# Performance work log

Hardware: AMD Instinct MI355X
Metric: run time of the kernel (lower is better)

## Reference

```python
import jax, jax.numpy as jnp
import numpy as np

B, NQ, NK, C, H = 4, 1024, 1024, 768, 12
DH = C // H
SCALE = DH ** -0.5
EPS = 1e-5  # nn.LayerNorm default
NEG_INF = float('-inf')


def _ln(x, g, b):
    m = jnp.mean(x, axis=-1, keepdims=True)
    v = jnp.mean((x - m) ** 2, axis=-1, keepdims=True)
    return (x - m) * jax.lax.rsqrt(v + EPS) * g + b


def _heads(t):  # [B,N,C] -> [B,H,N,Dh]
    Bq, N, _ = t.shape
    return t.reshape(Bq, N, H, DH).transpose(0, 2, 1, 3)


def setup_inputs() -> dict:
    key = jax.random.key(0)
    ks = jax.random.split(key, 32)
    w = lambda k, shape: jax.random.normal(k, shape, jnp.float32) * 0.02
    g = lambda k: 1.0 + jax.random.normal(k, (C,), jnp.float32) * 0.02
    b = lambda k: jax.random.normal(k, (C,), jnp.float32) * 0.02
    inp = {
        'x': jax.random.normal(ks[0], (B, NQ, C), jnp.float32),
        'y': jax.random.normal(ks[1], (B, NK, C), jnp.float32),
        'xpos': jnp.arange(B * NQ, dtype=jnp.int32).reshape(B, NQ),
        'ypos': jnp.arange(B * NK, dtype=jnp.int32).reshape(B, NK),
        'mask': jax.random.randint(ks[2], (NQ, NK), 0, 2) > 0,
        'similarities': jax.random.normal(ks[3], (B, H, NQ, NK), jnp.float32),
        # norms
        'ln1_g': g(ks[4]), 'ln1_b': b(ks[5]),
        'ln2_g': g(ks[6]), 'ln2_b': b(ks[7]),
        'ln3_g': g(ks[8]), 'ln3_b': b(ks[9]),
        'lny_g': g(ks[10]), 'lny_b': b(ks[11]),
        # self-attn (qkv_bias=False)
        'qkv_w': w(ks[12], (3 * C, C)),
        'aproj_w': w(ks[13], (C, C)), 'aproj_b': b(ks[14]),
        # cross-attn
        'pq_w': w(ks[15], (C, C)), 'pk_w': w(ks[16], (C, C)), 'pv_w': w(ks[17], (C, C)),
        'cproj_w': w(ks[18], (C, C)), 'cproj_b': b(ks[19]),
        # mlp (hidden = 4*C)
        'fc1_w': w(ks[20], (4 * C, C)), 'fc1_b': jax.random.normal(ks[21], (4 * C,), jnp.float32) * 0.02,
        'fc2_w': w(ks[22], (C, 4 * C)), 'fc2_b': b(ks[23]),
    }
    return inp


def reference(x, y, xpos, ypos, mask, similarities,
              ln1_g, ln1_b, ln2_g, ln2_b, ln3_g, ln3_b, lny_g, lny_b,
              qkv_w, aproj_w, aproj_b,
              pq_w, pk_w, pv_w, cproj_w, cproj_b,
              fc1_w, fc1_b, fc2_w, fc2_b):
    # ---- self-attention (rope=None, dropout=0) ----
    xn = _ln(x, ln1_g, ln1_b)
    qkv = (xn @ qkv_w.T).reshape(B, NQ, 3, H, DH).transpose(2, 0, 3, 1, 4)
    q, k, v = qkv[0], qkv[1], qkv[2]                       # [B,H,Nq,Dh]
    attn = jax.nn.softmax(jnp.einsum('bhqd,bhkd->bhqk', q, k) * SCALE, axis=-1)
    sa = jnp.einsum('bhqk,bhkd->bhqd', attn, v).transpose(0, 2, 1, 3).reshape(B, NQ, C)
    x = x + sa @ aproj_w.T + aproj_b

    # ---- sparse cross-attention with similarity bias + mask ----
    y_ = _ln(y, lny_g, lny_b)
    xn2 = _ln(x, ln2_g, ln2_b)
    cq = _heads(xn2 @ pq_w.T)                              # [B,H,Nq,Dh]
    ck = _heads(y_ @ pk_w.T)                               # [B,H,Nk,Dh]
    cv = _heads(y_ @ pv_w.T)
    scores = jnp.einsum('bhqd,bhkd->bhqk', cq, ck) * SCALE
    sims_c = similarities - jnp.mean(similarities, axis=1, keepdims=True)
    scores = scores + sims_c
    scores = jnp.where(mask[None, None], scores, NEG_INF)
    cattn = jax.nn.softmax(scores, axis=-1)
    ca = jnp.einsum('bhqk,bhkd->bhqd', cattn, cv).transpose(0, 2, 1, 3).reshape(B, NQ, C)
    x = x + ca @ cproj_w.T + cproj_b

    # ---- MLP (exact GELU, as nn.GELU default) ----
    xn3 = _ln(x, ln3_g, ln3_b)
    h = jax.nn.gelu(xn3 @ fc1_w.T + fc1_b, approximate=False)
    x = x + h @ fc2_w.T + fc2_b
    return (x, y)
```

## Files before the change

kernel.cpp:

```cpp
#include <hip/hip_runtime.h>
#include <cstdint>
#include <cstddef>


typedef __bf16 bf16;
typedef __attribute__((ext_vector_type(8))) __bf16 bf16x8;
typedef __attribute__((ext_vector_type(4))) __bf16 bf16x4;
typedef __attribute__((ext_vector_type(4))) float f32x4;

typedef __attribute__((address_space(1))) void gvoid;
typedef __attribute__((address_space(3))) void lvoid;

#define DEVI static __device__ __forceinline__

DEVI void gload16(const void* g, void* l) {
  __builtin_amdgcn_global_load_lds((gvoid*)(uintptr_t)g, (lvoid*)(uintptr_t)l, 16, 0, 0);
}

DEVI f32x4 mfma_bf16(bf16x8 a, bf16x8 b, f32x4 c) {
  return __builtin_amdgcn_mfma_f32_16x16x32_bf16(a, b, c, 0, 0, 0);
}

__global__ __launch_bounds__(256)
void bias_k(const float* __restrict__ sim,
            const unsigned char* __restrict__ mask,
            bf16* __restrict__ biasOut)
{
  __shared__ int red[4];
  const int blk = blockIdx.x;
  const int b = blk >> 10, q = blk & 1023;
  const int t = threadIdx.x;
  const int k4 = t * 4;

  int ds = mask[t * 4 + 1] + mask[t * 4 + 2] + mask[t * 4 + 3];
  #pragma unroll
  for (int o = 32; o; o >>= 1) ds += __shfl_xor(ds, o);
  if ((t & 63) == 0) red[t >> 6] = ds;
  __syncthreads();
  const int msh = ((red[0] + red[1] + red[2] + red[3]) == 0) ? 2 : 0;

  const float* sb = sim + (size_t)b * 12 * 1024 * 1024;
  bf16* ob = biasOut + (size_t)b * 12 * 1024 * 1024;

  f32x4 sv[12];
  f32x4 acc = {0.f, 0.f, 0.f, 0.f};
  #pragma unroll
  for (int h = 0; h < 12; ++h) {
    sv[h] = *(const f32x4*)(sb + ((size_t)h * 1024 + q) * 1024 + k4);
    acc += sv[h];
  }
  const f32x4 mean = acc * (1.0f / 12.0f);

  float mb[4];
  if (msh == 0) {
    const uchar4 mv = *(const uchar4*)(mask + (size_t)q * 1024 + k4);
    mb[0] = mv.x ? 0.f : -1e30f; mb[1] = mv.y ? 0.f : -1e30f;
    mb[2] = mv.z ? 0.f : -1e30f; mb[3] = mv.w ? 0.f : -1e30f;
  } else {
    const int4 mv = *(const int4*)((const int*)mask + (size_t)q * 1024 + k4);
    mb[0] = mv.x ? 0.f : -1e30f; mb[1] = mv.y ? 0.f : -1e30f;
    mb[2] = mv.z ? 0.f : -1e30f; mb[3] = mv.w ? 0.f : -1e30f;
  }

  #pragma unroll
  for (int h = 0; h < 12; ++h) {
    bf16x4 o;
    #pragma unroll
    for (int j = 0; j < 4; ++j)
      o[j] = (bf16)(sv[h][j] - mean[j] + mb[j]);
    *(bf16x4*)(ob + ((size_t)h * 1024 + q) * 1024 + k4) = o;
  }
}

struct CvtArgs {
  const float* src[8];
  bf16* dst[8];
  int end[8];
};
__global__ __launch_bounds__(256)
void cvt_all_k(CvtArgs a)
{
  const int i = blockIdx.x * 256 + threadIdx.x;
  int s = 0;
  #pragma unroll
  for (int j = 0; j < 7; ++j) s += (i >= a.end[j]) ? 1 : 0;
  const int base = s ? a.end[s - 1] : 0;
  const int off = i - base;
  const f32x4 v = *((const f32x4*)a.src[s] + off);
  bf16x4 o;
  o[0] = (bf16)v[0]; o[1] = (bf16)v[1]; o[2] = (bf16)v[2]; o[3] = (bf16)v[3];
  *(bf16x4*)(a.dst[s] + (size_t)off * 4) = o;
}

__global__ __launch_bounds__(256)
void copy4_k(const float* __restrict__ s, float* __restrict__ d, int n4)
{
  const int i = blockIdx.x * 256 + threadIdx.x;
  if (i < n4) ((f32x4*)d)[i] = ((const f32x4*)s)[i];
}

template<bool DUAL>
__global__ __launch_bounds__(256)
void ln_k(const float* __restrict__ inA, const float* __restrict__ gA,
          const float* __restrict__ bA, bf16* __restrict__ outA,
          const float* __restrict__ inB, const float* __restrict__ gB,
          const float* __restrict__ bB, bf16* __restrict__ outB)
{
  int row = blockIdx.x;
  const float* xin = inA; const float* g = gA; const float* be = bA; bf16* out = outA;
  if constexpr (DUAL) {
    if (row >= 4096) {
      row -= 4096; xin = inB; g = gB; be = bB; out = outB;
    }
  }
  const int tid = threadIdx.x;
  const int lane = tid & 63, w = tid >> 6;
  const float* xr = xin + (size_t)row * 768;
  const float v0 = xr[tid], v1 = xr[tid + 256], v2 = xr[tid + 512];
  float s = v0 + v1 + v2;
  #pragma unroll
  for (int o = 32; o; o >>= 1) s += __shfl_xor(s, o);
  __shared__ float r1[4], r2[4];
  if (lane == 0) r1[w] = s;
  __syncthreads();
  const float mean = (r1[0] + r1[1] + r1[2] + r1[3]) * (1.0f / 768.0f);
  const float d0 = v0 - mean, d1 = v1 - mean, d2 = v2 - mean;
  float q = d0 * d0 + d1 * d1 + d2 * d2;
  #pragma unroll
  for (int o = 32; o; o >>= 1) q += __shfl_xor(q, o);
  if (lane == 0) r2[w] = q;
  __syncthreads();
  const float inv = rsqrtf((r2[0] + r2[1] + r2[2] + r2[3]) * (1.0f / 768.0f) + 1e-5f);
  bf16* orow = out + (size_t)row * 768;
  orow[tid]       = (bf16)(d0 * inv * g[tid]       + be[tid]);
  orow[tid + 256] = (bf16)(d1 * inv * g[tid + 256] + be[tid + 256]);
  orow[tid + 512] = (bf16)(d2 * inv * g[tid + 512] + be[tid + 512]);
}

template<int BM, int BN, bool BIAS, bool GELU, bool RES, bool OBF, bool VT>
__global__ __launch_bounds__(256)
void gemm_bt(const bf16* __restrict__ A, const bf16* __restrict__ Bt,
             const float* __restrict__ bias, const float* __restrict__ res,
             bf16* __restrict__ Cb, float* __restrict__ Cf,
             bf16* __restrict__ vtOut, int vtBase,
             int nyPerXcd, int N, int K)
{
  constexpr int WM = BM / 2, WN = BN / 2;
  constexpr int FM = WM / 16, FN = WN / 16;
  __shared__ bf16 As[BM * 64];
  __shared__ bf16 Bs[BN * 64];
  const int f = blockIdx.x;
  const int xcd = f & 7, j = f >> 3;
  const int by = xcd + 8 * (j % nyPerXcd);
  const int bx = j / nyPerXcd;
  const int tid = threadIdx.x;
  const int lane = tid & 63;
  const int wv = tid >> 6;
  const int wr = wv >> 1, wc = wv & 1;
  const int l15 = lane & 15, lg = lane >> 4;
  const int bm = by * BM, bn = bx * BN;

  f32x4 acc[FM][FN];
  const f32x4 z = {0.f, 0.f, 0.f, 0.f};
  #pragma unroll
  for (int i = 0; i < FM; ++i)
    #pragma unroll
    for (int jj = 0; jj < FN; ++jj) acc[i][jj] = z;

  for (int k0 = 0; k0 < K; k0 += 64) {
    __syncthreads();
    #pragma unroll
    for (int c = tid; c < BM * 8; c += 256) {
      const int row = c >> 3, colb = (c & 7) << 4;
      gload16((const char*)A + ((size_t)(bm + row) * K + k0) * 2 + colb,
              (char*)As + (size_t)c * 16);
    }
    #pragma unroll
    for (int c = tid; c < BN * 8; c += 256) {
      const int row = c >> 3, colb = (c & 7) << 4;
      gload16((const char*)Bt + ((size_t)(bn + row) * K + k0) * 2 + colb,
              (char*)Bs + (size_t)c * 16);
    }
    __syncthreads();
    #pragma unroll
    for (int kk = 0; kk < 64; kk += 32) {
      bf16x8 af[FM], bfr[FN];
      #pragma unroll
      for (int mi = 0; mi < FM; ++mi)
        af[mi] = *(const bf16x8*)(As + (size_t)(wr * WM + mi * 16 + l15) * 64 + kk + lg * 8);
      #pragma unroll
      for (int ni = 0; ni < FN; ++ni)
        bfr[ni] = *(const bf16x8*)(Bs + (size_t)(wc * WN + ni * 16 + l15) * 64 + kk + lg * 8);
      #pragma unroll
      for (int mi = 0; mi < FM; ++mi)
        #pragma unroll
        for (int ni = 0; ni < FN; ++ni)
          acc[mi][ni] = mfma_bf16(af[mi], bfr[ni], acc[mi][ni]);
    }
  }

  #pragma unroll
  for (int mi = 0; mi < FM; ++mi) {
    const int row0 = bm + wr * WM + mi * 16 + lg * 4;
    #pragma unroll
    for (int ni = 0; ni < FN; ++ni) {
      const int col = bn + wc * WN + ni * 16 + l15;
      if constexpr (VT) {
        if (col >= vtBase) {
          const int hd = col - vtBase;
          const int bb = row0 >> 10, n0 = row0 & 1023;
          bf16x4 ov;
          #pragma unroll
          for (int r = 0; r < 4; ++r) ov[r] = (bf16)acc[mi][ni][r];
          *(bf16x4*)(vtOut + ((size_t)(bb * 768 + hd)) * 1024 + n0) = ov;
          continue;
        }
      }
      #pragma unroll
      for (int r = 0; r < 4; ++r) {
        float v = acc[mi][ni][r];
        if constexpr (BIAS) v += bias[col];
        if constexpr (GELU) v = 0.5f * v * (1.0f + erff(v * 0.70710678118654752f));
        if constexpr (RES)  v += res[(size_t)(row0 + r) * N + col];
        if constexpr (OBF)  Cb[(size_t)(row0 + r) * N + col] = (bf16)v;
        else                Cf[(size_t)(row0 + r) * N + col] = v;
      }
    }
  }
}

template<int CROSS>
__global__ __launch_bounds__(256, 3)
void fattn_k(const bf16* __restrict__ Qp, int ldq,
             const bf16* __restrict__ Kp, int ldk,
             const bf16* __restrict__ Vt,
             const bf16* __restrict__ bias,
             bf16* __restrict__ Out)
{
  __shared__ bf16 Kl[2][64 * 64];
  __shared__ bf16 Vl[2][64 * 64];
  __shared__ bf16 Pl[4][16 * 72];

  const int f = blockIdx.x;
  const int r8 = f & 7, rest = f >> 3;
  const int c6 = rest % 6, qt = rest / 6;
  const int pp = r8 + 8 * c6;
  const int b = pp / 12, hh = pp % 12;
  const int tid = threadIdx.x, lane = tid & 63, wq = tid >> 6;
  const int l15 = lane & 15, lg = lane >> 4;

  bf16x8 qreg0, qreg1;
  {
    const bf16* qsrc = Qp + (size_t)(b * 1024 + qt * 64 + wq * 16 + l15) * ldq + hh * 64 + lg * 8;
    qreg0 = *(const bf16x8*)qsrc;
    qreg1 = *(const bf16x8*)(qsrc + 32);
  }
  const char* Kbase = (const char*)(Kp + (size_t)b * 1024 * ldk + hh * 64);
  const char* Vbase = (const char*)(Vt + (size_t)(b * 12 + hh) * 64 * 1024);
  const bf16* biasRow = nullptr;
  if constexpr (CROSS)
    biasRow = bias + (((size_t)(b * 12 + hh)) * 1024 + qt * 64 + wq * 16 + l15) * 1024;

  f32x4 oacc[4];
  const f32x4 z = {0.f, 0.f, 0.f, 0.f};
  #pragma unroll
  for (int i = 0; i < 4; ++i) oacc[i] = z;
  float m_run = -1e30f, l_run = 0.f;

  char* PlW = (char*)&Pl[wq][0];
  const int swz = (l15 & 7) << 4;

  auto stage = [&](int buf, int t) {
    const int k0 = t * 64;
    #pragma unroll
    for (int jj = 0; jj < 2; ++jj) {
      const int c = jj * 256 + tid;
      const int r = c >> 3;
      const int sw = ((c & 7) ^ (r & 7)) << 4;
      gload16(Kbase + ((size_t)(k0 + r) * ldk) * 2 + sw, (char*)&Kl[buf][0] + (size_t)c * 16);
      gload16(Vbase + (size_t)r * 2048 + (size_t)k0 * 2 + sw, (char*)&Vl[buf][0] + (size_t)c * 16);
    }
  };

  stage(0, 0);
  __syncthreads();

  for (int t = 0; t < 16; ++t) {
    const int cur = t & 1;
    const int k0 = t * 64;
    if (t < 15) stage(cur ^ 1, t + 1);

    bf16x4 bv[4];
    if constexpr (CROSS) {
      const bf16* bp = biasRow + k0 + lg * 4;
      #pragma unroll
      for (int ni = 0; ni < 4; ++ni) bv[ni] = *(const bf16x4*)(bp + ni * 16);
    }

    f32x4 sacc[4];
    #pragma unroll
    for (int i = 0; i < 4; ++i) sacc[i] = z;
    #pragma unroll
    for (int ni = 0; ni < 4; ++ni) {
      const int rowb = (ni * 16 + l15) * 128;
      const bf16x8 a0 = *(const bf16x8*)((char*)&Kl[cur][0] + rowb + ((lg * 16) ^ swz));
      const bf16x8 a1 = *(const bf16x8*)((char*)&Kl[cur][0] + rowb + ((64 + lg * 16) ^ swz));
      sacc[ni] = mfma_bf16(a0, qreg0, sacc[ni]);
      sacc[ni] = mfma_bf16(a1, qreg1, sacc[ni]);
    }

    float sv[16];
    #pragma unroll
    for (int ni = 0; ni < 4; ++ni)
      #pragma unroll
      for (int r = 0; r < 4; ++r)
        sv[ni * 4 + r] = sacc[ni][r] * 0.125f;
    if constexpr (CROSS) {
      #pragma unroll
      for (int ni = 0; ni < 4; ++ni)
        #pragma unroll
        for (int r = 0; r < 4; ++r)
          sv[ni * 4 + r] += (float)bv[ni][r];
    }
    float mx = sv[0];
    #pragma unroll
    for (int jj = 1; jj < 16; ++jj) mx = fmaxf(mx, sv[jj]);
    mx = fmaxf(mx, __shfl_xor(mx, 16));
    mx = fmaxf(mx, __shfl_xor(mx, 32));
    const float mnew = fmaxf(m_run, mx);
    const float corr = __expf(m_run - mnew);
    m_run = mnew;
    float ps = 0.f;
    #pragma unroll
    for (int jj = 0; jj < 16; ++jj) { sv[jj] = __expf(sv[jj] - mnew); ps += sv[jj]; }
    l_run = l_run * corr + ps;

    #pragma unroll
    for (int ni = 0; ni < 4; ++ni) {
      bf16x4 pw;
      #pragma unroll
      for (int r = 0; r < 4; ++r) pw[r] = (bf16)sv[ni * 4 + r];
      *(bf16x4*)(PlW + l15 * 144 + ni * 32 + lg * 8) = pw;
    }
    float cr[4];
    #pragma unroll
    for (int r = 0; r < 4; ++r) cr[r] = __shfl(corr, ((lane >> 4) << 2) + r);
    #pragma unroll
    for (int nd = 0; nd < 4; ++nd)
      #pragma unroll
      for (int r = 0; r < 4; ++r) oacc[nd][r] *= cr[r];

    const bf16x8 p0 = *(const bf16x8*)(PlW + l15 * 144 + lg * 16);
    const bf16x8 p1 = *(const bf16x8*)(PlW + l15 * 144 + 64 + lg * 16);
    #pragma unroll
    for (int nd = 0; nd < 4; ++nd) {
      const int rowb = (nd * 16 + l15) * 128;
      const bf16x8 v0 = *(const bf16x8*)((char*)&Vl[cur][0] + rowb + ((lg * 16) ^ swz));
      const bf16x8 v1 = *(const bf16x8*)((char*)&Vl[cur][0] + rowb + ((64 + lg * 16) ^ swz));
      oacc[nd] = mfma_bf16(p0, v0, oacc[nd]);
      oacc[nd] = mfma_bf16(p1, v1, oacc[nd]);
    }
    __syncthreads();
  }

  float ls = l_run + __shfl_xor(l_run, 16);
  ls += __shfl_xor(ls, 32);
  const float inv = 1.0f / ls;
  float ivr[4];
  #pragma unroll
  for (int r = 0; r < 4; ++r) ivr[r] = __shfl(inv, ((lane >> 4) << 2) + r);
  bf16* ob = Out + (size_t)(b * 1024 + qt * 64 + wq * 16 + lg * 4) * 768 + hh * 64 + l15;
  #pragma unroll
  for (int r = 0; r < 4; ++r)
    #pragma unroll
    for (int nd = 0; nd < 4; ++nd)
      ob[(size_t)r * 768 + nd * 16] = (bf16)(oacc[nd][r] * ivr[r]);
}

extern "C" void kernel_launch(void* const* d_in, const int* in_sizes, int n_in,
                              void* d_out, int out_size, void* d_ws, size_t ws_size,
                              hipStream_t stream)
{
  (void)in_sizes; (void)n_in; (void)out_size; (void)ws_size;
  const float* x    = (const float*)d_in[0];
  const float* y    = (const float*)d_in[1];
  const unsigned char* mask = (const unsigned char*)d_in[4];
  const float* sim  = (const float*)d_in[5];
  const float* ln1g = (const float*)d_in[6];
  const float* ln1b = (const float*)d_in[7];
  const float* ln2g = (const float*)d_in[8];
  const float* ln2b = (const float*)d_in[9];
  const float* ln3g = (const float*)d_in[10];
  const float* ln3b = (const float*)d_in[11];
  const float* lnyg = (const float*)d_in[12];
  const float* lnyb = (const float*)d_in[13];
  const float* qkvw = (const float*)d_in[14];
  const float* apw  = (const float*)d_in[15];
  const float* apb  = (const float*)d_in[16];
  const float* pqw  = (const float*)d_in[17];
  const float* pkw  = (const float*)d_in[18];
  const float* pvw  = (const float*)d_in[19];
  const float* cpw  = (const float*)d_in[20];
  const float* cpb  = (const float*)d_in[21];
  const float* f1w  = (const float*)d_in[22];
  const float* f1b  = (const float*)d_in[23];
  const float* f2w  = (const float*)d_in[24];
  const float* f2b  = (const float*)d_in[25];

  char* ws = (char*)d_ws;
  size_t off = 0;
  auto alloc = [&](size_t bytes) -> void* {
    off = (off + 255) & ~(size_t)255;
    void* p = ws + off;
    off += bytes;
    return p;
  };
  const size_t T = 4096;
  bf16* w_qkv = (bf16*)alloc((size_t)2304 * 768 * 2);
  bf16* w_ap  = (bf16*)alloc((size_t)768 * 768 * 2);
  bf16* w_pq  = (bf16*)alloc((size_t)768 * 768 * 2);
  bf16* w_pkv = (bf16*)alloc((size_t)1536 * 768 * 2);
  bf16* w_cp  = (bf16*)alloc((size_t)768 * 768 * 2);
  bf16* w_f1  = (bf16*)alloc((size_t)3072 * 768 * 2);
  bf16* w_f2  = (bf16*)alloc((size_t)768 * 3072 * 2);
  bf16* xn    = (bf16*)alloc(T * 768 * 2);
  bf16* qkvo  = (bf16*)alloc(T * 2304 * 2);
  bf16* vt    = (bf16*)alloc((size_t)48 * 64 * 1024 * 2);
  bf16* sa    = (bf16*)alloc(T * 768 * 2);
  float* x1   = (float*)alloc(T * 768 * 4);
  bf16* yln   = (bf16*)alloc(T * 768 * 2);
  bf16* xn2   = (bf16*)alloc(T * 768 * 2);
  bf16* cqf   = (bf16*)alloc(T * 768 * 2);
  bf16* ckv   = (bf16*)alloc(T * 1536 * 2);
  bf16* cvtT  = (bf16*)alloc((size_t)48 * 64 * 1024 * 2);
  bf16* biasA = (bf16*)alloc((size_t)4 * 12 * 1024 * 1024 * 2);
  bf16* ca    = (bf16*)alloc(T * 768 * 2);
  float* x2   = (float*)alloc(T * 768 * 4);
  bf16* xn3   = (bf16*)alloc(T * 768 * 2);
  bf16* hbuf  = (bf16*)alloc(T * 3072 * 2);

  {
    CvtArgs a;
    const float* srcs[8] = {qkvw, apw, pqw, pkw, pvw, cpw, f1w, f2w};
    bf16* dsts[8] = {w_qkv, w_ap, w_pq, w_pkv, w_pkv + 768 * 768, w_cp, w_f1, w_f2};
    const int n4s[8] = {442368, 147456, 147456, 147456, 147456, 147456, 589824, 589824};
    int cum = 0;
    for (int j = 0; j < 8; ++j) {
      a.src[j] = srcs[j]; a.dst[j] = dsts[j];
      cum += n4s[j]; a.end[j] = cum;
    }
    cvt_all_k<<<cum / 256, 256, 0, stream>>>(a);
  }

  bias_k<<<4096, 256, 0, stream>>>(sim, mask, biasA);

  ln_k<true><<<8192, 256, 0, stream>>>(x, ln1g, ln1b, xn, y, lnyg, lnyb, yln);
  gemm_bt<128,128,false,false,false,true,true><<<576, 256, 0, stream>>>(
      xn, w_qkv, nullptr, nullptr, qkvo, nullptr, vt, 1536, 4, 2304, 768);
  fattn_k<0><<<768, 256, 0, stream>>>(
      qkvo, 2304, qkvo + 768, 2304, vt, nullptr, sa);
  gemm_bt<64,128,true,false,true,false,false><<<384, 256, 0, stream>>>(
      sa, w_ap, apb, x, nullptr, x1, nullptr, 0, 8, 768, 768);

  ln_k<false><<<4096, 256, 0, stream>>>(x1, ln2g, ln2b, xn2,
                                        nullptr, nullptr, nullptr, nullptr);
  gemm_bt<64,128,false,false,false,true,false><<<384, 256, 0, stream>>>(
      xn2, w_pq, nullptr, nullptr, cqf, nullptr, nullptr, 0, 8, 768, 768);
  gemm_bt<128,128,false,false,false,true,true><<<384, 256, 0, stream>>>(
      yln, w_pkv, nullptr, nullptr, ckv, nullptr, cvtT, 768, 4, 1536, 768);
  fattn_k<1><<<768, 256, 0, stream>>>(
      cqf, 768, ckv, 1536, cvtT, biasA, ca);
  gemm_bt<64,128,true,false,true,false,false><<<384, 256, 0, stream>>>(
      ca, w_cp, cpb, x1, nullptr, x2, nullptr, 0, 8, 768, 768);

  ln_k<false><<<4096, 256, 0, stream>>>(x2, ln3g, ln3b, xn3,
                                        nullptr, nullptr, nullptr, nullptr);
  gemm_bt<128,128,true,true,false,true,false><<<768, 256, 0, stream>>>(
      xn3, w_f1, f1b, nullptr, hbuf, nullptr, nullptr, 0, 4, 3072, 768);
  gemm_bt<64,128,true,false,true,false,false><<<384, 256, 0, stream>>>(
      hbuf, w_f2, f2b, x2, nullptr, (float*)d_out, nullptr, 0, 8, 768, 3072);

  copy4_k<<<3072, 256, 0, stream>>>(y, (float*)d_out + 3145728, 786432);
}
```

Measured before the change: 388.6 us.

## Merge independent kernels into combined launches to fill the GPU

Several independent kernels now share a launch, with branches on block index. Weight conversion and both LayerNorms run as one prep kernel, the QKV GEMM runs alongside the similarity-bias kernel, the attention projection GEMM runs with the K/V projection GEMM, and FC2 runs with the y copy. The aim is to cut launch count and fill the tail of small-grid GEMMs with other independent work. The cost is heterogeneous blocks and a shared-memory size set by the largest branch, which may lower occupancy for the lighter blocks.

```diff
diff --git a/kernel.cpp b/kernel.cpp
--- a/kernel.cpp
+++ b/kernel.cpp
@@ -21,138 +21,16 @@
   return __builtin_amdgcn_mfma_f32_16x16x32_bf16(a, b, c, 0, 0, 0);
 }
 
-__global__ __launch_bounds__(256)
-void bias_k(const float* __restrict__ sim,
-            const unsigned char* __restrict__ mask,
-            bf16* __restrict__ biasOut)
-{
-  __shared__ int red[4];
-  const int blk = blockIdx.x;
-  const int b = blk >> 10, q = blk & 1023;
-  const int t = threadIdx.x;
-  const int k4 = t * 4;
-
-  int ds = mask[t * 4 + 1] + mask[t * 4 + 2] + mask[t * 4 + 3];
-  #pragma unroll
-  for (int o = 32; o; o >>= 1) ds += __shfl_xor(ds, o);
-  if ((t & 63) == 0) red[t >> 6] = ds;
-  __syncthreads();
-  const int msh = ((red[0] + red[1] + red[2] + red[3]) == 0) ? 2 : 0;
-
-  const float* sb = sim + (size_t)b * 12 * 1024 * 1024;
-  bf16* ob = biasOut + (size_t)b * 12 * 1024 * 1024;
-
-  f32x4 sv[12];
-  f32x4 acc = {0.f, 0.f, 0.f, 0.f};
-  #pragma unroll
-  for (int h = 0; h < 12; ++h) {
-    sv[h] = *(const f32x4*)(sb + ((size_t)h * 1024 + q) * 1024 + k4);
-    acc += sv[h];
-  }
-  const f32x4 mean = acc * (1.0f / 12.0f);
-
-  float mb[4];
-  if (msh == 0) {
-    const uchar4 mv = *(const uchar4*)(mask + (size_t)q * 1024 + k4);
-    mb[0] = mv.x ? 0.f : -1e30f; mb[1] = mv.y ? 0.f : -1e30f;
-    mb[2] = mv.z ? 0.f : -1e30f; mb[3] = mv.w ? 0.f : -1e30f;
-  } else {
-    const int4 mv = *(const int4*)((const int*)mask + (size_t)q * 1024 + k4);
-    mb[0] = mv.x ? 0.f : -1e30f; mb[1] = mv.y ? 0.f : -1e30f;
-    mb[2] = mv.z ? 0.f : -1e30f; mb[3] = mv.w ? 0.f : -1e30f;
-  }
-
-  #pragma unroll
-  for (int h = 0; h < 12; ++h) {
-    bf16x4 o;
-    #pragma unroll
-    for (int j = 0; j < 4; ++j)
-      o[j] = (bf16)(sv[h][j] - mean[j] + mb[j]);
-    *(bf16x4*)(ob + ((size_t)h * 1024 + q) * 1024 + k4) = o;
-  }
-}
-
-struct CvtArgs {
-  const float* src[8];
-  bf16* dst[8];
-  int end[8];
-};
-__global__ __launch_bounds__(256)
-void cvt_all_k(CvtArgs a)
-{
-  const int i = blockIdx.x * 256 + threadIdx.x;
-  int s = 0;
-  #pragma unroll
-  for (int j = 0; j < 7; ++j) s += (i >= a.end[j]) ? 1 : 0;
-  const int base = s ? a.end[s - 1] : 0;
-  const int off = i - base;
-  const f32x4 v = *((const f32x4*)a.src[s] + off);
-  bf16x4 o;
-  o[0] = (bf16)v[0]; o[1] = (bf16)v[1]; o[2] = (bf16)v[2]; o[3] = (bf16)v[3];
-  *(bf16x4*)(a.dst[s] + (size_t)off * 4) = o;
-}
-
-__global__ __launch_bounds__(256)
-void copy4_k(const float* __restrict__ s, float* __restrict__ d, int n4)
-{
-  const int i = blockIdx.x * 256 + threadIdx.x;
-  if (i < n4) ((f32x4*)d)[i] = ((const f32x4*)s)[i];
-}
-
-template<bool DUAL>
-__global__ __launch_bounds__(256)
-void ln_k(const float* __restrict__ inA, const float* __restrict__ gA,
-          const float* __restrict__ bA, bf16* __restrict__ outA,
-          const float* __restrict__ inB, const float* __restrict__ gB,
-          const float* __restrict__ bB, bf16* __restrict__ outB)
-{
-  int row = blockIdx.x;
-  const float* xin = inA; const float* g = gA; const float* be = bA; bf16* out = outA;
-  if constexpr (DUAL) {
-    if (row >= 4096) {
-      row -= 4096; xin = inB; g = gB; be = bB; out = outB;
-    }
-  }
-  const int tid = threadIdx.x;
-  const int lane = tid & 63, w = tid >> 6;
-  const float* xr = xin + (size_t)row * 768;
-  const float v0 = xr[tid], v1 = xr[tid + 256], v2 = xr[tid + 512];
-  float s = v0 + v1 + v2;
-  #pragma unroll
-  for (int o = 32; o; o >>= 1) s += __shfl_xor(s, o);
-  __shared__ float r1[4], r2[4];
-  if (lane == 0) r1[w] = s;
-  __syncthreads();
-  const float mean = (r1[0] + r1[1] + r1[2] + r1[3]) * (1.0f / 768.0f);
-  const float d0 = v0 - mean, d1 = v1 - mean, d2 = v2 - mean;
-  float q = d0 * d0 + d1 * d1 + d2 * d2;
-  #pragma unroll
-  for (int o = 32; o; o >>= 1) q += __shfl_xor(q, o);
-  if (lane == 0) r2[w] = q;
-  __syncthreads();
-  const float inv = rsqrtf((r2[0] + r2[1] + r2[2] + r2[3]) * (1.0f / 768.0f) + 1e-5f);
-  bf16* orow = out + (size_t)row * 768;
-  orow[tid]       = (bf16)(d0 * inv * g[tid]       + be[tid]);
-  orow[tid + 256] = (bf16)(d1 * inv * g[tid + 256] + be[tid + 256]);
-  orow[tid + 512] = (bf16)(d2 * inv * g[tid + 512] + be[tid + 512]);
-}
 
 template<int BM, int BN, bool BIAS, bool GELU, bool RES, bool OBF, bool VT>
-__global__ __launch_bounds__(256)
-void gemm_bt(const bf16* __restrict__ A, const bf16* __restrict__ Bt,
-             const float* __restrict__ bias, const float* __restrict__ res,
-             bf16* __restrict__ Cb, float* __restrict__ Cf,
-             bf16* __restrict__ vtOut, int vtBase,
-             int nyPerXcd, int N, int K)
+DEVI void gemm_dev(bf16* As, bf16* Bs, int by, int bx,
+                   const bf16* __restrict__ A, const bf16* __restrict__ Bt,
+                   const float* __restrict__ bias, const float* __restrict__ res,
+                   bf16* __restrict__ Cb, float* __restrict__ Cf,
+                   bf16* __restrict__ vtOut, int vtBase, int N, int K)
 {
   constexpr int WM = BM / 2, WN = BN / 2;
   constexpr int FM = WM / 16, FN = WN / 16;
-  __shared__ bf16 As[BM * 64];
-  __shared__ bf16 Bs[BN * 64];
-  const int f = blockIdx.x;
-  const int xcd = f & 7, j = f >> 3;
-  const int by = xcd + 8 * (j % nyPerXcd);
-  const int bx = j / nyPerXcd;
   const int tid = threadIdx.x;
   const int lane = tid & 63;
   const int wv = tid >> 6;
@@ -227,6 +105,208 @@
       }
     }
   }
+}
+
+DEVI void bias_dev(int blk, int* red,
+                   const float* __restrict__ sim,
+                   const unsigned char* __restrict__ mask,
+                   bf16* __restrict__ biasOut)
+{
+  const int b = blk >> 10, q = blk & 1023;
+  const int t = threadIdx.x;
+  const int k4 = t * 4;
+
+  int ds = mask[t * 4 + 1] + mask[t * 4 + 2] + mask[t * 4 + 3];
+  #pragma unroll
+  for (int o = 32; o; o >>= 1) ds += __shfl_xor(ds, o);
+  if ((t & 63) == 0) red[t >> 6] = ds;
+  __syncthreads();
+  const int msh = ((red[0] + red[1] + red[2] + red[3]) == 0) ? 2 : 0;
+
+  const float* sb = sim + (size_t)b * 12 * 1024 * 1024;
+  bf16* ob = biasOut + (size_t)b * 12 * 1024 * 1024;
+
+  f32x4 sv[12];
+  f32x4 acc = {0.f, 0.f, 0.f, 0.f};
+  #pragma unroll
+  for (int h = 0; h < 12; ++h) {
+    sv[h] = *(const f32x4*)(sb + ((size_t)h * 1024 + q) * 1024 + k4);
+    acc += sv[h];
+  }
+  const f32x4 mean = acc * (1.0f / 12.0f);
+
+  float mb[4];
+  if (msh == 0) {
+    const uchar4 mv = *(const uchar4*)(mask + (size_t)q * 1024 + k4);
+    mb[0] = mv.x ? 0.f : -1e30f; mb[1] = mv.y ? 0.f : -1e30f;
+    mb[2] = mv.z ? 0.f : -1e30f; mb[3] = mv.w ? 0.f : -1e30f;
+  } else {
+    const int4 mv = *(const int4*)((const int*)mask + (size_t)q * 1024 + k4);
+    mb[0] = mv.x ? 0.f : -1e30f; mb[1] = mv.y ? 0.f : -1e30f;
+    mb[2] = mv.z ? 0.f : -1e30f; mb[3] = mv.w ? 0.f : -1e30f;
+  }
+
+  #pragma unroll
+  for (int h = 0; h < 12; ++h) {
+    bf16x4 o;
+    #pragma unroll
+    for (int j = 0; j < 4; ++j)
+      o[j] = (bf16)(sv[h][j] - mean[j] + mb[j]);
+    *(bf16x4*)(ob + ((size_t)h * 1024 + q) * 1024 + k4) = o;
+  }
+}
+
+DEVI void ln_dev(int row, float* r1, float* r2,
+                 const float* __restrict__ xin, const float* __restrict__ g,
+                 const float* __restrict__ be, bf16* __restrict__ out)
+{
+  const int tid = threadIdx.x;
+  const int lane = tid & 63, w = tid >> 6;
+  const float* xr = xin + (size_t)row * 768;
+  const float v0 = xr[tid], v1 = xr[tid + 256], v2 = xr[tid + 512];
+  float s = v0 + v1 + v2;
+  #pragma unroll
+  for (int o = 32; o; o >>= 1) s += __shfl_xor(s, o);
+  if (lane == 0) r1[w] = s;
+  __syncthreads();
+  const float mean = (r1[0] + r1[1] + r1[2] + r1[3]) * (1.0f / 768.0f);
+  const float d0 = v0 - mean, d1 = v1 - mean, d2 = v2 - mean;
+  float q = d0 * d0 + d1 * d1 + d2 * d2;
+  #pragma unroll
+  for (int o = 32; o; o >>= 1) q += __shfl_xor(q, o);
+  if (lane == 0) r2[w] = q;
+  __syncthreads();
+  const float inv = rsqrtf((r2[0] + r2[1] + r2[2] + r2[3]) * (1.0f / 768.0f) + 1e-5f);
+  bf16* orow = out + (size_t)row * 768;
+  orow[tid]       = (bf16)(d0 * inv * g[tid]       + be[tid]);
+  orow[tid + 256] = (bf16)(d1 * inv * g[tid + 256] + be[tid + 256]);
+  orow[tid + 512] = (bf16)(d2 * inv * g[tid + 512] + be[tid + 512]);
+}
+
+
+struct CvtArgs {
+  const float* src[8];
+  bf16* dst[8];
+  int end[8];
+};
+
+__global__ __launch_bounds__(256)
+void prep_k(CvtArgs a,
+            const float* __restrict__ x, const float* __restrict__ g1,
+            const float* __restrict__ b1, bf16* __restrict__ xn,
+            const float* __restrict__ y, const float* __restrict__ gy,
+            const float* __restrict__ by_, bf16* __restrict__ yln)
+{
+  __shared__ float r1[4], r2[4];
+  const int f = blockIdx.x;
+  if (f < 9216) {
+    const int i = f * 256 + threadIdx.x;
+    int s = 0;
+    #pragma unroll
+    for (int j = 0; j < 7; ++j) s += (i >= a.end[j]) ? 1 : 0;
+    const int base = s ? a.end[s - 1] : 0;
+    const int off = i - base;
+    const f32x4 v = *((const f32x4*)a.src[s] + off);
+    bf16x4 o;
+    o[0] = (bf16)v[0]; o[1] = (bf16)v[1]; o[2] = (bf16)v[2]; o[3] = (bf16)v[3];
+    *(bf16x4*)(a.dst[s] + (size_t)off * 4) = o;
+  } else if (f < 13312) {
+    ln_dev(f - 9216, r1, r2, x, g1, b1, xn);
+  } else {
+    ln_dev(f - 13312, r1, r2, y, gy, by_, yln);
+  }
+}
+
+__global__ __launch_bounds__(256)
+void qkvbias_k(const bf16* __restrict__ xn, const bf16* __restrict__ w_qkv,
+               bf16* __restrict__ qkvo, bf16* __restrict__ vt,
+               const float* __restrict__ sim, const unsigned char* __restrict__ mask,
+               bf16* __restrict__ biasA)
+{
+  __shared__ bf16 As[128 * 64];
+  __shared__ bf16 Bs[128 * 64];
+  const int f = blockIdx.x;
+  if (f < 576) {
+    const int xcd = f & 7, j = f >> 3;
+    const int by = xcd + 8 * (j % 4);
+    const int bx = j / 4;
+    gemm_dev<128,128,false,false,false,true,true>(As, Bs, by, bx,
+        xn, w_qkv, nullptr, nullptr, qkvo, nullptr, vt, 1536, 2304, 768);
+  } else {
+    bias_dev(f - 576, (int*)As, sim, mask, biasA);
+  }
+}
+
+__global__ __launch_bounds__(256)
+void apkv_k(const bf16* __restrict__ sa, const bf16* __restrict__ w_ap,
+            const float* __restrict__ apb, const float* __restrict__ x,
+            float* __restrict__ x1,
+            const bf16* __restrict__ yln, const bf16* __restrict__ w_pkv,
+            bf16* __restrict__ ckv, bf16* __restrict__ cvtT)
+{
+  __shared__ bf16 As[128 * 64];
+  __shared__ bf16 Bs[128 * 64];
+  const int f = blockIdx.x;
+  if (f < 384) {
+    const int xcd = f & 7, j = f >> 3;
+    const int by = xcd + 8 * (j % 8);
+    const int bx = j / 8;
+    gemm_dev<64,128,true,false,true,false,false>(As, Bs, by, bx,
+        sa, w_ap, apb, x, nullptr, x1, nullptr, 0, 768, 768);
+  } else {
+    const int g = f - 384;
+    const int xcd = g & 7, j = g >> 3;
+    const int by = xcd + 8 * (j % 4);
+    const int bx = j / 4;
+    gemm_dev<128,128,false,false,false,true,true>(As, Bs, by, bx,
+        yln, w_pkv, nullptr, nullptr, ckv, nullptr, cvtT, 768, 1536, 768);
+  }
+}
+
+__global__ __launch_bounds__(256)
+void fc2copy_k(const bf16* __restrict__ hbuf, const bf16* __restrict__ w_f2,
+               const float* __restrict__ f2b, const float* __restrict__ x2,
+               float* __restrict__ outp,
+               const float* __restrict__ y, float* __restrict__ ycopy)
+{
+  __shared__ bf16 As[128 * 64];
+  __shared__ bf16 Bs[128 * 64];
+  const int f = blockIdx.x;
+  if (f < 384) {
+    const int xcd = f & 7, j = f >> 3;
+    const int by = xcd + 8 * (j % 8);
+    const int bx = j / 8;
+    gemm_dev<64,128,true,false,true,false,false>(As, Bs, by, bx,
+        hbuf, w_f2, f2b, x2, nullptr, outp, nullptr, 0, 768, 3072);
+  } else {
+    for (int i = (f - 384) * 256 + threadIdx.x; i < 786432; i += 512 * 256)
+      ((f32x4*)ycopy)[i] = ((const f32x4*)y)[i];
+  }
+}
+
+template<int BM, int BN, bool BIAS, bool GELU, bool RES, bool OBF>
+__global__ __launch_bounds__(256)
+void gemm_bt(const bf16* __restrict__ A, const bf16* __restrict__ Bt,
+             const float* __restrict__ bias, const float* __restrict__ res,
+             bf16* __restrict__ Cb, float* __restrict__ Cf,
+             int nyPerXcd, int N, int K)
+{
+  __shared__ bf16 As[BM * 64];
+  __shared__ bf16 Bs[BN * 64];
+  const int f = blockIdx.x;
+  const int xcd = f & 7, j = f >> 3;
+  const int by = xcd + 8 * (j % nyPerXcd);
+  const int bx = j / nyPerXcd;
+  gemm_dev<BM,BN,BIAS,GELU,RES,OBF,false>(As, Bs, by, bx,
+      A, Bt, bias, res, Cb, Cf, nullptr, 0, N, K);
+}
+
+__global__ __launch_bounds__(256)
+void ln_k(const float* __restrict__ xin, const float* __restrict__ g,
+          const float* __restrict__ be, bf16* __restrict__ out)
+{
+  __shared__ float r1[4], r2[4];
+  ln_dev(blockIdx.x, r1, r2, xin, g, be, out);
 }
 
 template<int CROSS>
@@ -439,8 +519,8 @@
   bf16* xn3   = (bf16*)alloc(T * 768 * 2);
   bf16* hbuf  = (bf16*)alloc(T * 3072 * 2);
 
+  CvtArgs a;
   {
-    CvtArgs a;
     const float* srcs[8] = {qkvw, apw, pqw, pkw, pvw, cpw, f1w, f2w};
     bf16* dsts[8] = {w_qkv, w_ap, w_pq, w_pkv, w_pkv + 768 * 768, w_cp, w_f1, w_f2};
     const int n4s[8] = {442368, 147456, 147456, 147456, 147456, 147456, 589824, 589824};
@@ -449,36 +529,33 @@
       a.src[j] = srcs[j]; a.dst[j] = dsts[j];
       cum += n4s[j]; a.end[j] = cum;
     }
-    cvt_all_k<<<cum / 256, 256, 0, stream>>>(a);
-  }
-
-  bias_k<<<4096, 256, 0, stream>>>(sim, mask, biasA);
-
-  ln_k<true><<<8192, 256, 0, stream>>>(x, ln1g, ln1b, xn, y, lnyg, lnyb, yln);
-  gemm_bt<128,128,false,false,false,true,true><<<576, 256, 0, stream>>>(
-      xn, w_qkv, nullptr, nullptr, qkvo, nullptr, vt, 1536, 4, 2304, 768);
+  }
+
+  prep_k<<<17408, 256, 0, stream>>>(a, x, ln1g, ln1b, xn, y, lnyg, lnyb, yln);
+
+  qkvbias_k<<<4672, 256, 0, stream>>>(xn, w_qkv, qkvo, vt, sim, mask, biasA);
+
   fattn_k<0><<<768, 256, 0, stream>>>(
       qkvo, 2304, qkvo + 768, 2304, vt, nullptr, sa);
-  gemm_bt<64,128,true,false,true,false,false><<<384, 256, 0, stream>>>(
-      sa, w_ap, apb, x, nullptr, x1, nullptr, 0, 8, 768, 768);
-
-  ln_k<false><<<4096, 256, 0, stream>>>(x1, ln2g, ln2b, xn2,
-                                        nullptr, nullptr, nullptr, nullptr);
-  gemm_bt<64,128,false,false,false,true,false><<<384, 256, 0, stream>>>(
-      xn2, w_pq, nullptr, nullptr, cqf, nullptr, nullptr, 0, 8, 768, 768);
-  gemm_bt<128,128,false,false,false,true,true><<<384, 256, 0, stream>>>(
-      yln, w_pkv, nullptr, nullptr, ckv, nullptr, cvtT, 768, 4, 1536, 768);
+
+  apkv_k<<<768, 256, 0, stream>>>(sa, w_ap, apb, x, x1, yln, w_pkv, ckv, cvtT);
+
+  ln_k<<<4096, 256, 0, stream>>>(x1, ln2g, ln2b, xn2);
+
+  gemm_bt<64,128,false,false,false,true><<<384, 256, 0, stream>>>(
+      xn2, w_pq, nullptr, nullptr, cqf, nullptr, 8, 768, 768);
+
   fattn_k<1><<<768, 256, 0, stream>>>(
       cqf, 768, ckv, 1536, cvtT, biasA, ca);
-  gemm_bt<64,128,true,false,true,false,false><<<384, 256, 0, stream>>>(
-      ca, w_cp, cpb, x1, nullptr, x2, nullptr, 0, 8, 768, 768);
-
-  ln_k<false><<<4096, 256, 0, stream>>>(x2, ln3g, ln3b, xn3,
-                                        nullptr, nullptr, nullptr, nullptr);
-  gemm_bt<128,128,true,true,false,true,false><<<768, 256, 0, stream>>>(
-      xn3, w_f1, f1b, nullptr, hbuf, nullptr, nullptr, 0, 4, 3072, 768);
-  gemm_bt<64,128,true,false,true,false,false><<<384, 256, 0, stream>>>(
-      hbuf, w_f2, f2b, x2, nullptr, (float*)d_out, nullptr, 0, 8, 768, 3072);
-
-  copy4_k<<<3072, 256, 0, stream>>>(y, (float*)d_out + 3145728, 786432);
-}
+
+  gemm_bt<64,128,true,false,true,false><<<384, 256, 0, stream>>>(
+      ca, w_cp, cpb, x1, nullptr, x2, 8, 768, 768);
+
+  ln_k<<<4096, 256, 0, stream>>>(x2, ln3g, ln3b, xn3);
+
+  gemm_bt<128,128,true,true,false,true><<<768, 256, 0, stream>>>(
+      xn3, w_f1, f1b, nullptr, hbuf, nullptr, 4, 3072, 768);
+
+  fc2copy_k<<<896, 256, 0, stream>>>(
+      hbuf, w_f2, f2b, x2, (float*)d_out, y, (float*)d_out + 3145728);
+}
```

Measured after the change: 380.7 us. 1.02x faster.
